# Optimization experiments

Hardware: AMD Instinct MI355X
Metric: run time of the kernel (lower is better)

The kernel has to match this reference:

```python
import jax, jax.numpy as jnp
import numpy as np

N0, N1, N2 = 1500, 6000, 4000
F_IN, F_OUT = 32, 32
K00, K0P = 2, 2
K1N, K11, K12, K1P = 2, 2, 2, 2
K2N, K22 = 2, 2


def chebyshev(L, k, x):
    # Chebyshev recursion: T1 = L x, T2 = 2 L T1 - x, T_j = 2 L T_{j-1} - T_{j-2}
    # Returns (n, F, k) stack of T1..Tk (identity term handled by caller).
    t_prev = L @ x
    terms = [t_prev]
    t_pp = x
    for _ in range(k - 1):
        t = 2.0 * (L @ t_prev) - t_pp
        t_pp, t_prev = t_prev, t
        terms.append(t)
    return jnp.stack(terms, axis=2)


def _sym(key, n):
    a = jax.random.normal(key, (n, n), jnp.float32) / jnp.sqrt(jnp.float32(n))
    return 0.5 * (a + a.T)


def setup_inputs():
    key = jax.random.key(0)
    ks = jax.random.split(key, 16)
    x0 = jax.random.normal(ks[0], (N0, F_IN), jnp.float32)
    x1 = jax.random.normal(ks[1], (N1, F_IN), jnp.float32)
    x2 = jax.random.normal(ks[2], (N2, F_IN), jnp.float32)
    B1 = jax.random.normal(ks[3], (N0, N1), jnp.float32) / jnp.sqrt(jnp.float32(N1))
    B2 = jax.random.normal(ks[4], (N1, N2), jnp.float32) / jnp.sqrt(jnp.float32(N2))
    L0 = _sym(ks[5], N0)
    L1l = _sym(ks[6], N1)
    L1u = _sym(ks[7], N1)
    L2 = _sym(ks[8], N2)
    # Degree matrices: diagonal with strictly positive entries (as in real SC data).
    D1 = jnp.diag(jax.random.uniform(ks[9], (N0,), jnp.float32, 0.5, 2.0))
    D2 = jnp.diag(jax.random.uniform(ks[10], (N1,), jnp.float32, 0.5, 2.0))
    D3 = jnp.diag(jax.random.uniform(ks[11], (N2,), jnp.float32, 0.5, 2.0))
    D5 = jnp.diag(jax.random.uniform(ks[12], (N1,), jnp.float32, 0.5, 2.0))
    W0 = jax.random.normal(ks[13], (F_IN, F_OUT, 1 + K00 + 1 + K0P), jnp.float32) * 0.05
    W1 = jax.random.normal(ks[14], (F_IN, F_OUT, 1 + K1N + 1 + K11 + K12 + 1 + K1P), jnp.float32) * 0.05
    W2 = jax.random.normal(ks[15], (F_IN, F_OUT, 1 + K2N + 1 + K22), jnp.float32) * 0.05
    return dict(x0=x0, x1=x1, x2=x2, B1=B1, B2=B2, L0=L0, L1l=L1l, L1u=L1u,
                L2=L2, D1=D1, D2=D2, D3=D3, D5=D5, W0=W0, W1=W1, W2=W2)


def _forward(x0, x1, x2, B1, B2, L0, L1l, L1u, L2, d1_inv, d2, d3, d5_pinv, W0, W1, W2):
    # ---- order 0 ----
    x0p = d1_inv[:, None] * (B1 @ x1)               # inv(D1) @ B1 @ x1
    X0 = jnp.concatenate([x0[:, :, None], chebyshev(L0, K00, x0),
                          x0p[:, :, None], chebyshev(L0, K0P, x0p)], axis=2)
    # ---- order 1 ----
    x1n = d2[:, None] * (B1.T @ (d1_inv[:, None] * x0))  # D2 @ B1.T @ inv(D1) @ x0
    x1p = B2 @ (d3[:, None] * x2)                        # B2 @ D3 @ x2
    X1 = jnp.concatenate([x1n[:, :, None], chebyshev(L1l, K1N, x1n),
                          x1[:, :, None], chebyshev(L1l, K11, x1), chebyshev(L1u, K12, x1),
                          x1p[:, :, None], chebyshev(L1u, K1P, x1p)], axis=2)
    # ---- order 2 ----
    x2n = B2.T @ (d5_pinv[:, None] * x1)                 # B2.T @ pinv(D5) @ x1
    X2 = jnp.concatenate([x2n[:, :, None], chebyshev(L2, K2N, x2n),
                          x2[:, :, None], chebyshev(L2, K22, x2)], axis=2)
    y0 = jax.nn.relu(jnp.einsum('nik,iok->no', X0, W0))
    y1 = jax.nn.relu(jnp.einsum('nik,iok->no', X1, W1))
    y2 = jax.nn.relu(jnp.einsum('nik,iok->no', X2, W2))
    return (y0, y1, y2)


def reference(x0, x1, x2, B1, B2, L0, L1l, L1u, L2, D1, D2, D3, D5, W0, W1, W2):
    # D matrices are diagonal degree matrices; inverse/pinverse of a diagonal
    # matrix is the diagonal of (safe) reciprocals -- identical math to
    # torch.inverse / torch.pinverse on these inputs, without an O(n^3) solve.
    d1_inv = 1.0 / jnp.diag(D1)
    d2 = jnp.diag(D2)
    d3 = jnp.diag(D3)
    d5 = jnp.diag(D5)
    d5_pinv = jnp.where(d5 != 0, 1.0 / d5, 0.0)
    return _forward(x0, x1, x2, B1, B2, L0, L1l, L1u, L2, d1_inv, d2, d3, d5_pinv, W0, W1, W2)
```

## Files before the change

### kernel.cpp

```cpp
#include <hip/hip_runtime.h>
#include <stdint.h>

typedef __attribute__((ext_vector_type(4))) float f32x4;
typedef __attribute__((ext_vector_type(8))) short s16x8;
typedef unsigned short us;

static __device__ __forceinline__ us f2bf(float f) {
  union { float f; uint32_t u; } v; v.f = f;
  uint32_t u = v.u;
  u += 0x7fffu + ((u >> 16) & 1u);
  return (us)(u >> 16);
}

static __device__ __forceinline__ float dval(const float* dv, long r, long dstr, int mode) {
  if (!dv || mode == 0) return 1.f;
  float d = dv[r * dstr];
  if (mode == 2) return (d != 0.f) ? 1.f / d : 0.f;
  return d;
}

static __device__ void tpose_tile(const float* __restrict__ src, long lds_, int n,
                                  const float* __restrict__ dv, long dstr, int mode,
                                  us* __restrict__ dst, int ldn, int tile,
                                  us (*sm)[72]) {
  const int t = threadIdx.x;
  const int r0 = tile * 64;
  {
    const int rr = t & 63;
    const int cg = t >> 6;
    const int gr = r0 + rr;
    float sc = 1.f;
    f32x4 v0 = {0.f, 0.f, 0.f, 0.f}, v1 = {0.f, 0.f, 0.f, 0.f};
    if (gr < n) {
      sc = dval(dv, gr, dstr, mode);
      const float* sp = src + (long)gr * lds_ + cg * 8;
      v0 = *(const f32x4*)sp;
      v1 = *(const f32x4*)(sp + 4);
    }
#pragma unroll
    for (int j = 0; j < 4; ++j) {
      sm[cg * 8 + j][rr] = f2bf(v0[j] * sc);
      sm[cg * 8 + 4 + j][rr] = f2bf(v1[j] * sc);
    }
  }
  __syncthreads();
  {
    const int f = t >> 3;
    const int nc = (t & 7) * 8;
    if (r0 + nc < ldn) {
      s16x8 v = *(const s16x8*)&sm[f][nc];
      *(s16x8*)(dst + (size_t)f * ldn + r0 + nc) = v;
    }
  }
}

static __device__ void convT_tile(const float* __restrict__ in, int ldi, int nI, int nC,
                                  us* __restrict__ outT, int ldoT, int bx, int by,
                                  us (*sT)[72]) {
  const int t = threadIdx.x;
  const int tc0 = bx * 64;
  const int tr0 = by * 64;
  const int c0 = (t & 15) * 4;
  const int r0 = (t >> 4) * 4;
  us ub[4][4];
#pragma unroll
  for (int j = 0; j < 4; ++j) {
    int gr = tr0 + r0 + j;
    f32x4 v = {0.f, 0.f, 0.f, 0.f};
    if (gr < nI) {
      const float* pI = in + (size_t)gr * ldi + tc0 + c0;
      if (tc0 + c0 + 3 < nC) {
        v = *(const f32x4*)pI;
      } else {
#pragma unroll
        for (int jj = 0; jj < 4; ++jj) if (tc0 + c0 + jj < nC) v[jj] = pI[jj];
      }
    }
#pragma unroll
    for (int jj = 0; jj < 4; ++jj) ub[j][jj] = f2bf(v[jj]);
  }
#pragma unroll
  for (int jj = 0; jj < 4; ++jj) {
    union { us u[4]; unsigned long long ll; } w;
#pragma unroll
    for (int j = 0; j < 4; ++j) w.u[j] = ub[j][jj];
    *(unsigned long long*)&sT[c0 + jj][r0] = w.ll;
  }
  __syncthreads();
#pragma unroll
  for (int p = 0; p < 2; ++p) {
    int orow = (t >> 3) + p * 32;
    int rcol = (t & 7) * 8;
    int grow = tc0 + orow;
    int gcol = tr0 + rcol;
    if (grow < nC && gcol < ldoT) {
      union { unsigned long long ll[2]; s16x8 v; } w;
      w.ll[0] = *(const unsigned long long*)&sT[orow][rcol];
      w.ll[1] = *(const unsigned long long*)&sT[orow][rcol + 4];
      *(s16x8*)(outT + (size_t)grow * ldoT + gcol) = w.v;
    }
  }
}

struct TSeg { const float* src; us* dst; int lds_, n, ldn, start; };
struct TPack { TSeg t[8]; int nseg; };

__global__ __launch_bounds__(256) void tpose_batch(TPack P) {
  __shared__ us sm[32][72];
  int b = blockIdx.x;
  int si = P.nseg - 1;
  while (si > 0 && P.t[si].start > b) --si;
  const TSeg s = P.t[si];
  tpose_tile(s.src, s.lds_, s.n, nullptr, 0, 0, s.dst, s.ldn, b - s.start, sm);
}

__global__ __launch_bounds__(256) void prep(
    const float* __restrict__ x0, const float* __restrict__ x1, const float* __restrict__ x2,
    const float* __restrict__ D1, const float* __restrict__ D3, const float* __restrict__ D5,
    const float* __restrict__ W0, const float* __restrict__ W1, const float* __restrict__ W2,
    us* x0T, us* x0dT, us* x1T, us* x1dT, us* x2T, us* x2dT,
    us* W0T, us* W1T, us* W2T,
    float* __restrict__ X0a, float* __restrict__ X1a, float* __restrict__ X2a) {
  __shared__ us sm[32][72];
  int b = blockIdx.x;
  if (b < 24)  { tpose_tile(x0, 32, 1500, nullptr, 0, 0, x0T, 1536, b, sm); return; }
  b -= 24;
  if (b < 24)  { tpose_tile(x0, 32, 1500, D1, 1501, 2, x0dT, 1536, b, sm); return; }
  b -= 24;
  if (b < 94)  { tpose_tile(x1, 32, 6000, nullptr, 0, 0, x1T, 6016, b, sm); return; }
  b -= 94;
  if (b < 94)  { tpose_tile(x1, 32, 6000, D5, 6001, 2, x1dT, 6016, b, sm); return; }
  b -= 94;
  if (b < 63)  { tpose_tile(x2, 32, 4000, nullptr, 0, 0, x2T, 4032, b, sm); return; }
  b -= 63;
  if (b < 63)  { tpose_tile(x2, 32, 4000, D3, 4001, 1, x2dT, 4032, b, sm); return; }
  b -= 63;
  if (b < 3) {
    const float* W = (b == 0) ? W0 : ((b == 1) ? W1 : W2);
    us* dst = (b == 0) ? W0T : ((b == 1) ? W1T : W2T);
    const int K = (b == 1) ? 11 : 6;
    const int C = K * 32;
    const int CP = (b == 1) ? 384 : 192;
    for (int idx = threadIdx.x; idx < 32 * CP; idx += 256) {
      int o = idx / CP, j = idx - o * CP;
      float v = 0.f;
      if (j < C) { int k = j >> 5, i = j & 31; v = W[((long)i * 32 + o) * K + k]; }
      dst[(size_t)o * CP + j] = f2bf(v);
    }
    return;
  }
  b -= 3;
  const long V0 = 1500L * 48, V1 = 6000L * 88, V2 = 4000L * 48;
  for (long i = (long)b * 256 + threadIdx.x; i < V0 + V1 + V2; i += 512L * 256) {
    f32x4 v = {0.f, 0.f, 0.f, 0.f};
    float* dst;
    if (i < V0) {
      long r = i / 48; int c0 = (int)(i - r * 48) * 4;
      if (c0 < 32) v = *(const f32x4*)(x0 + r * 32 + c0);
      dst = X0a + r * 192 + c0;
    } else if (i < V0 + V1) {
      long j = i - V0; long r = j / 88; int c0 = (int)(j - r * 88) * 4;
      if (c0 >= 96 && c0 < 128) v = *(const f32x4*)(x1 + r * 32 + (c0 - 96));
      dst = X1a + r * 352 + c0;
    } else {
      long j = i - V0 - V1; long r = j / 48; int c0 = (int)(j - r * 48) * 4;
      if (c0 >= 96 && c0 < 128) v = *(const f32x4*)(x2 + r * 32 + (c0 - 96));
      dst = X2a + r * 192 + c0;
    }
    *(f32x4*)dst = v;
  }
}

struct Seg {
  const void* A; us* Aout;
  const us* Bt0; const us* Bt1;
  const float* S0; const float* S1; const float* sv;
  float* C0; float* C1;
  float alpha, beta;
  int lda, ldao, ldS, sstr, ldc;
  int n_rows, n_k, ldb, smode, kchunk, tiles, ky, start;
};
struct CSeg { const float* in; us* out; int ldi, nI, nC, ldoT, cx, start; };
struct Mega {
  Seg s[4]; CSeg c[2]; TSeg t[2];
  int nseg, gemm_end, nconv, conv_end, ntp;
};

template <int F, bool RELU, typename AT>
__global__ __launch_bounds__(256) void mega(Mega P) {
  __shared__ __align__(16) us lds[64 * 128];
  const int b = blockIdx.x;
  if (b >= P.gemm_end) {
    if (b < P.conv_end) {
      int lb = b - P.gemm_end;
      int si = P.nconv - 1;
      while (si > 0 && P.c[si].start > lb) --si;
      const CSeg s = P.c[si];
      int l = lb - s.start;
      convT_tile(s.in, s.ldi, s.nI, s.nC, s.out, s.ldoT, l % s.cx, l / s.cx, (us(*)[72])lds);
    } else {
      int lb = b - P.conv_end;
      int si = P.ntp - 1;
      while (si > 0 && P.t[si].start > lb) --si;
      const TSeg s = P.t[si];
      tpose_tile(s.src, s.lds_, s.n, nullptr, 0, 0, s.dst, s.ldn, lb - s.start, (us(*)[72])lds);
    }
    return;
  }

  us* sA = lds;
  us* sX = lds + 64 * 64;

  int si = P.nseg - 1;
  while (si > 0 && P.s[si].start > b) --si;
  const Seg sg = P.s[si];
  const int local = b - sg.start;
  const int bx = local % sg.tiles;
  const int kidx = local / sg.tiles;

  const AT* __restrict__ A = (const AT*)sg.A;
  const int n_rows = sg.n_rows, n_k = sg.n_k, ldb = sg.ldb;

  const int tid = threadIdx.x;
  const int k_begin = kidx * sg.kchunk;
  const int k_end = min(n_k, k_begin + sg.kchunk);
  const int nsteps = (k_end - k_begin + 63) >> 6;

  const int srow = tid >> 2;
  const int sslot = tid & 3;
  const int kc_off = sslot * 16;
  const long arowg = (long)bx * 64 + srow;
  const bool arow_ok = arowg < n_rows;
  const bool xrow_ok = (F == 64) || (srow < 32);
  const us* xbase = ((srow < 32) ? sg.Bt0 : sg.Bt1) + (size_t)(srow & 31) * ldb;

  s16x8 abf0 = (s16x8)0, abf1 = (s16x8)0;
  f32x4 af0, af1, af2, af3;
  s16x8 x0r = (s16x8)0, x1r = (s16x8)0;

  auto load_tiles = [&](int k0) {
    int kc = k0 + kc_off;
    if constexpr (sizeof(AT) == 4) {
      af0 = f32x4{0, 0, 0, 0}; af1 = af0; af2 = af0; af3 = af0;
      if (arow_ok) {
        const float* ap = (const float*)A + (size_t)arowg * sg.lda + kc;
        if (kc + 15 < n_k) {
          af0 = *(const f32x4*)ap; af1 = *(const f32x4*)(ap + 4);
          af2 = *(const f32x4*)(ap + 8); af3 = *(const f32x4*)(ap + 12);
        } else {
#pragma unroll
          for (int j = 0; j < 4; ++j) {
            if (kc + j < n_k) af0[j] = ap[j];
            if (kc + 4 + j < n_k) af1[j] = ap[4 + j];
            if (kc + 8 + j < n_k) af2[j] = ap[8 + j];
            if (kc + 12 + j < n_k) af3[j] = ap[12 + j];
          }
        }
      }
    } else {
      abf0 = (s16x8)0; abf1 = (s16x8)0;
      if (arow_ok) {
        const us* ap = (const us*)A + (size_t)arowg * sg.lda + kc;
        if (kc + 15 < n_k) {
          abf0 = *(const s16x8*)ap; abf1 = *(const s16x8*)(ap + 8);
        } else {
#pragma unroll
          for (int j = 0; j < 8; ++j) {
            if (kc + j < n_k) abf0[j] = (short)ap[j];
            if (kc + 8 + j < n_k) abf1[j] = (short)ap[8 + j];
          }
        }
      }
    }
    if (xrow_ok) {
      x0r = *(const s16x8*)(xbase + kc);
      x1r = *(const s16x8*)(xbase + kc + 8);
    }
  };

  load_tiles(k_begin);

  const int wave = tid >> 6;
  const int lane = tid & 63;
  const int g = lane >> 4;
  const int r = lane & 15;
  const int wslot0 = ((2 * sslot) ^ (srow & 7)) * 8;
  const int wslot1 = ((2 * sslot + 1) ^ (srow & 7)) * 8;

  f32x4 acc[F / 16];
#pragma unroll
  for (int i = 0; i < F / 16; ++i) acc[i] = f32x4{0.f, 0.f, 0.f, 0.f};

  for (int s = 0; s < nsteps; ++s) {
    s16x8 pk0, pk1;
    if constexpr (sizeof(AT) == 4) {
#pragma unroll
      for (int j = 0; j < 4; ++j) {
        pk0[j] = (short)f2bf(af0[j]); pk0[4 + j] = (short)f2bf(af1[j]);
        pk1[j] = (short)f2bf(af2[j]); pk1[4 + j] = (short)f2bf(af3[j]);
      }
      if (sg.Aout && arow_ok) {
        us* q = sg.Aout + (size_t)arowg * sg.ldao + (k_begin + s * 64 + kc_off);
        *(s16x8*)q = pk0;
        *(s16x8*)(q + 8) = pk1;
      }
    } else { pk0 = abf0; pk1 = abf1; }
    *(s16x8*)&sA[srow * 64 + wslot0] = pk0;
    *(s16x8*)&sA[srow * 64 + wslot1] = pk1;
    if (xrow_ok) {
      *(s16x8*)&sX[srow * 64 + wslot0] = x0r;
      *(s16x8*)&sX[srow * 64 + wslot1] = x1r;
    }
    __syncthreads();
    if (s + 1 < nsteps) load_tiles(k_begin + (s + 1) * 64);

    const int arow = wave * 16 + r;
#pragma unroll
    for (int kk = 0; kk < 2; ++kk) {
      s16x8 afr = *(s16x8*)&sA[arow * 64 + (((kk * 4 + g) ^ (arow & 7)) << 3)];
#pragma unroll
      for (int nt = 0; nt < F / 16; ++nt) {
        int xc = nt * 16 + r;
        s16x8 bfr = *(s16x8*)&sX[xc * 64 + (((kk * 4 + g) ^ (xc & 7)) << 3)];
        acc[nt] = __builtin_amdgcn_mfma_f32_16x16x32_bf16(afr, bfr, acc[nt], 0, 0, 0);
      }
    }
    __syncthreads();
  }

  float svv[4];
#pragma unroll
  for (int j = 0; j < 4; ++j) {
    long row = (long)bx * 64 + wave * 16 + g * 4 + j;
    svv[j] = (row < n_rows) ? dval(sg.sv, row, sg.sstr, sg.smode) : 0.f;
  }
#pragma unroll
  for (int nt = 0; nt < F / 16; ++nt) {
    float* C = (F == 64 && nt >= 2) ? sg.C1 : sg.C0;
    const float* S = (F == 64 && nt >= 2) ? sg.S1 : sg.S0;
    int col = ((F == 64) ? (nt & 1) : nt) * 16 + r;
#pragma unroll
    for (int j = 0; j < 4; ++j) {
      long row = (long)bx * 64 + wave * 16 + g * 4 + j;
      if (row < n_rows) {
        float v = sg.alpha * acc[nt][j] * svv[j];
        if (S && (sg.ky == 1 || kidx == 0)) v += sg.beta * S[row * (size_t)sg.ldS + col];
        if (sg.ky > 1) {
          atomicAdd(&C[row * (size_t)sg.ldc + col], v);
        } else {
          if (RELU) v = fmaxf(v, 0.0f);
          C[row * (size_t)sg.ldc + col] = v;
        }
      }
    }
  }
}

__global__ void colcopy(float* __restrict__ dst, const float* __restrict__ src, int n,
                        const float* __restrict__ dv, long dstr, int mode) {
  int idx = blockIdx.x * 256 + threadIdx.x;
  if (idx >= n * 32) return;
  dst[idx] = src[idx] * dval(dv, idx >> 5, dstr, mode);
}
__global__ void scale_ld(float* __restrict__ dst, long ld, int n,
                         const float* __restrict__ dv, long dstr, int mode) {
  int idx = blockIdx.x * 256 + threadIdx.x;
  if (idx >= n * 32) return;
  dst[(size_t)(idx >> 5) * ld + (idx & 31)] *= dval(dv, idx >> 5, dstr, mode);
}
__global__ __launch_bounds__(256) void mm_at(
    const float* __restrict__ A, int lda, int m,
    const float* __restrict__ X,
    float* __restrict__ C, int ldc, int n, int kchunk) {
  const int fg = threadIdx.x & 3;
  const int cg = threadIdx.x >> 2;
  const int c = blockIdx.x * 256 + cg * 4;
  const int k0 = blockIdx.y * kchunk;
  const int k1 = min(m, k0 + kchunk);
  const int f = fg * 8;
  float acc[4][8];
#pragma unroll
  for (int a = 0; a < 4; ++a)
#pragma unroll
    for (int b = 0; b < 8; ++b) acc[a][b] = 0.f;
  for (int k = k0; k < k1; ++k) {
    const float* Ar = A + (size_t)k * lda + c;
    f32x4 a;
    if (c + 3 < n) a = *(const f32x4*)Ar;
    else {
      a = f32x4{0.f, 0.f, 0.f, 0.f};
#pragma unroll
      for (int j = 0; j < 4; ++j) if (c + j < n) a[j] = Ar[j];
    }
    f32x4 xa = *(const f32x4*)(X + (size_t)k * 32 + f);
    f32x4 xb = *(const f32x4*)(X + (size_t)k * 32 + f + 4);
#pragma unroll
    for (int cc = 0; cc < 4; ++cc)
#pragma unroll
      for (int jj = 0; jj < 4; ++jj) {
        acc[cc][jj] += a[cc] * xa[jj];
        acc[cc][4 + jj] += a[cc] * xb[jj];
      }
  }
  if (c >= n) return;
#pragma unroll
  for (int cc = 0; cc < 4; ++cc) {
    if (c + cc >= n) break;
#pragma unroll
    for (int jj = 0; jj < 8; ++jj)
      atomicAdd(&C[(size_t)(c + cc) * ldc + f + jj], acc[cc][jj]);
  }
}


extern "C" void kernel_launch(void* const* d_in, const int* in_sizes, int n_in,
                              void* d_out, int out_size, void* d_ws, size_t ws_size,
                              hipStream_t stream) {
  (void)in_sizes; (void)n_in; (void)out_size;
  const float* x0  = (const float*)d_in[0];
  const float* x1  = (const float*)d_in[1];
  const float* x2  = (const float*)d_in[2];
  const float* B1  = (const float*)d_in[3];
  const float* B2  = (const float*)d_in[4];
  const float* L0  = (const float*)d_in[5];
  const float* L1l = (const float*)d_in[6];
  const float* L1u = (const float*)d_in[7];
  const float* L2  = (const float*)d_in[8];
  const float* D1  = (const float*)d_in[9];
  const float* D2  = (const float*)d_in[10];
  const float* D3  = (const float*)d_in[11];
  const float* D5  = (const float*)d_in[12];
  const float* W0  = (const float*)d_in[13];
  const float* W1  = (const float*)d_in[14];
  const float* W2  = (const float*)d_in[15];
  float* out = (float*)d_out;

  char* p = (char*)d_ws;
  auto alloc = [&](size_t b) { char* r = p; p += (b + 255) & ~(size_t)255; return r; };

  us* x0T   = (us*)alloc((size_t)32 * 1536 * 2);
  us* x0dT  = (us*)alloc((size_t)32 * 1536 * 2);
  us* x1T   = (us*)alloc((size_t)32 * 6016 * 2);
  us* x1dT  = (us*)alloc((size_t)32 * 6016 * 2);
  us* x2T   = (us*)alloc((size_t)32 * 4032 * 2);
  us* x2dT  = (us*)alloc((size_t)32 * 4032 * 2);
  us* x0pT  = (us*)alloc((size_t)32 * 1536 * 2);
  us* x1nT  = (us*)alloc((size_t)32 * 6016 * 2);
  us* x1pT  = (us*)alloc((size_t)32 * 6016 * 2);
  us* x2nT  = (us*)alloc((size_t)32 * 4032 * 2);
  us* T1a0T = (us*)alloc((size_t)32 * 1536 * 2);
  us* T1b0T = (us*)alloc((size_t)32 * 1536 * 2);
  us* T1laT = (us*)alloc((size_t)32 * 6016 * 2);
  us* T1lbT = (us*)alloc((size_t)32 * 6016 * 2);
  us* T1uaT = (us*)alloc((size_t)32 * 6016 * 2);
  us* T1ubT = (us*)alloc((size_t)32 * 6016 * 2);
  us* T1a2T = (us*)alloc((size_t)32 * 4032 * 2);
  us* T1b2T = (us*)alloc((size_t)32 * 4032 * 2);
  us* W0T   = (us*)alloc((size_t)32 * 192 * 2);
  us* W1T   = (us*)alloc((size_t)32 * 384 * 2);
  us* W2T   = (us*)alloc((size_t)32 * 192 * 2);

  float* X0a = (float*)alloc((size_t)1500 * 192 * 4);
  float* X1a = (float*)alloc((size_t)6000 * 352 * 4);
  float* X2a = (float*)alloc((size_t)4000 * 192 * 4);

  float* z0  = (float*)alloc((size_t)1500 * 32 * 4);
  float* sx1 = (float*)alloc((size_t)6000 * 32 * 4);

  size_t used = (size_t)(p - (char*)d_ws);
  const size_t needB  = (size_t)6000 * 1536 * 2 + (size_t)4000 * 6016 * 2 + 1024;
  const size_t needL1 = 2 * (size_t)6000 * 6016 * 2 + 1024;
  const size_t needL02 = (size_t)1500 * 1536 * 2 + (size_t)4000 * 4032 * 2 + 1024;
  bool haveB = used + needB <= ws_size;
  int tier = 0;
  if (haveB) {
    if (used + needB + needL1 + needL02 <= ws_size) tier = 2;
    else if (used + needB + needL1 <= ws_size) tier = 1;
  }
  us *B1t = nullptr, *B2t = nullptr;
  us *L0bf = nullptr, *L1lbf = nullptr, *L1ubf = nullptr, *L2bf = nullptr;
  if (haveB) {
    B1t = (us*)alloc((size_t)6000 * 1536 * 2);
    B2t = (us*)alloc((size_t)4000 * 6016 * 2);
  }
  if (tier >= 1) {
    L1lbf = (us*)alloc((size_t)6000 * 6016 * 2);
    L1ubf = (us*)alloc((size_t)6000 * 6016 * 2);
  }
  if (tier >= 2) {
    L0bf = (us*)alloc((size_t)1500 * 1536 * 2);
    L2bf = (us*)alloc((size_t)4000 * 4032 * 2);
  }

  auto nb = [](long t) { return (unsigned)((t + 255) / 256); };
  auto seg = [](const void* A, us* Aout, int lda, int ldao, int n_rows, int n_k,
                const us* Bt0, const us* Bt1, int ldb,
                float alpha, const float* S0, const float* S1, int ldS, float beta,
                const float* sv, int sstr, int smode,
                float* C0, float* C1, int ldc,
                int kchunk, int tiles, int ky, int start) {
    Seg s;
    s.A = A; s.Aout = Aout; s.Bt0 = Bt0; s.Bt1 = Bt1; s.S0 = S0; s.S1 = S1; s.sv = sv;
    s.C0 = C0; s.C1 = C1; s.alpha = alpha; s.beta = beta;
    s.lda = lda; s.ldao = ldao; s.ldS = ldS; s.sstr = sstr; s.ldc = ldc;
    s.n_rows = n_rows; s.n_k = n_k; s.ldb = ldb; s.smode = smode;
    s.kchunk = kchunk; s.tiles = tiles; s.ky = ky; s.start = start;
    return s;
  };

  prep<<<877, 256, 0, stream>>>(x0, x1, x2, D1, D3, D5, W0, W1, W2,
                                x0T, x0dT, x1T, x1dT, x2T, x2dT, W0T, W1T, W2T,
                                X0a, X1a, X2a);

  {
    Mega P{};
    P.nseg = 2;
    P.s[0] = seg(B1, nullptr, 6000, 0, 1500, 6000, x1T, x1T, 6016,
                 1.f, nullptr, nullptr, 0, 0.f, D1, 1501, 2,
                 X0a + 3 * 32, nullptr, 192, 768, 24, 8, 0);
    P.s[1] = seg(B2, nullptr, 4000, 0, 6000, 4000, x2dT, x2dT, 4032,
                 1.f, nullptr, nullptr, 0, 0.f, nullptr, 0, 0,
                 X1a + 8 * 32, nullptr, 352, 512, 94, 8, 192);
    P.gemm_end = 944;
    if (haveB) {
      P.nconv = 2;
      P.c[0] = CSeg{B1, B1t, 6000, 1500, 6000, 1536, 94, 0};
      P.c[1] = CSeg{B2, B2t, 4000, 6000, 4000, 6016, 63, 2256};
      P.conv_end = 944 + 8178;
    } else {
      P.nconv = 0; P.conv_end = 944;
    }
    P.ntp = 0;
    mega<32, false, float><<<P.conv_end, 256, 0, stream>>>(P);
  }

  if (haveB) {
    Mega P{};
    P.nseg = 2;
    P.s[0] = seg(B1t, nullptr, 1536, 0, 6000, 1536, x0dT, x0dT, 1536,
                 1.f, nullptr, nullptr, 0, 0.f, D2, 6001, 1,
                 X1a + 0 * 32, nullptr, 352, 384, 94, 4, 0);
    P.s[1] = seg(B2t, nullptr, 6016, 0, 4000, 6016, x1dT, x1dT, 6016,
                 1.f, nullptr, nullptr, 0, 0.f, nullptr, 0, 0,
                 X2a + 0 * 32, nullptr, 192, 768, 63, 8, 376);
    P.gemm_end = 880;
    P.nconv = 0; P.conv_end = 880;
    P.ntp = 2;
    P.t[0] = TSeg{X0a + 3 * 32, x0pT, 192, 1500, 1536, 0};
    P.t[1] = TSeg{X1a + 8 * 32, x1pT, 352, 6000, 6016, 24};
    mega<32, false, us><<<998, 256, 0, stream>>>(P);
  } else {
    colcopy<<<nb(1500L * 32), 256, 0, stream>>>(z0, x0, 1500, D1, 1501, 2);
    mm_at<<<dim3(24, 24), 256, 0, stream>>>(B1, 6000, 1500, z0, X1a + 0 * 32, 352, 6000, 63);
    scale_ld<<<nb(6000L * 32), 256, 0, stream>>>(X1a + 0 * 32, 352, 6000, D2, 6001, 1);
    colcopy<<<nb(6000L * 32), 256, 0, stream>>>(sx1, x1, 6000, D5, 6001, 2);
    mm_at<<<dim3(16, 32), 256, 0, stream>>>(B2, 4000, 6000, sx1, X2a + 0 * 32, 192, 4000, 188);
    TPack T{};
    T.nseg = 2;
    T.t[0] = TSeg{X0a + 3 * 32, x0pT, 192, 1500, 1536, 0};
    T.t[1] = TSeg{X1a + 8 * 32, x1pT, 352, 6000, 6016, 24};
    tpose_batch<<<118, 256, 0, stream>>>(T);
  }

  {
    TPack T{};
    T.nseg = 2;
    T.t[0] = TSeg{X1a + 0 * 32, x1nT, 352, 6000, 6016, 0};
    T.t[1] = TSeg{X2a + 0 * 32, x2nT, 192, 4000, 4032, 94};
    tpose_batch<<<157, 256, 0, stream>>>(T);
  }

  {
    Mega P{};
    P.nseg = 4;
    P.s[0] = seg(L0, L0bf, 1500, 1536, 1500, 1500, x0T, x0pT, 1536,
                 1.f, nullptr, nullptr, 0, 0.f, nullptr, 0, 0,
                 X0a + 1 * 32, X0a + 4 * 32, 192, 384, 24, 4, 0);
    P.s[1] = seg(L1l, L1lbf, 6000, 6016, 6000, 6000, x1nT, x1T, 6016,
                 1.f, nullptr, nullptr, 0, 0.f, nullptr, 0, 0,
                 X1a + 1 * 32, X1a + 4 * 32, 352, 768, 94, 8, 96);
    P.s[2] = seg(L1u, L1ubf, 6000, 6016, 6000, 6000, x1T, x1pT, 6016,
                 1.f, nullptr, nullptr, 0, 0.f, nullptr, 0, 0,
                 X1a + 6 * 32, X1a + 9 * 32, 352, 768, 94, 8, 848);
    P.s[3] = seg(L2, L2bf, 4000, 4032, 4000, 4000, x2nT, x2T, 4032,
                 1.f, nullptr, nullptr, 0, 0.f, nullptr, 0, 0,
                 X2a + 1 * 32, X2a + 4 * 32, 192, 512, 63, 8, 1600);
    P.gemm_end = 2104; P.nconv = 0; P.conv_end = 2104; P.ntp = 0;
    mega<64, false, float><<<2104, 256, 0, stream>>>(P);
  }

  {
    TPack T{};
    T.nseg = 8;
    T.t[0] = TSeg{X0a + 1 * 32, T1a0T, 192, 1500, 1536, 0};
    T.t[1] = TSeg{X0a + 4 * 32, T1b0T, 192, 1500, 1536, 24};
    T.t[2] = TSeg{X1a + 1 * 32, T1laT, 352, 6000, 6016, 48};
    T.t[3] = TSeg{X1a + 4 * 32, T1lbT, 352, 6000, 6016, 142};
    T.t[4] = TSeg{X1a + 6 * 32, T1uaT, 352, 6000, 6016, 236};
    T.t[5] = TSeg{X1a + 9 * 32, T1ubT, 352, 6000, 6016, 330};
    T.t[6] = TSeg{X2a + 1 * 32, T1a2T, 192, 4000, 4032, 424};
    T.t[7] = TSeg{X2a + 4 * 32, T1b2T, 192, 4000, 4032, 487};
    tpose_batch<<<550, 256, 0, stream>>>(T);
  }

  {
    if (tier == 2) {
      Mega P{};
      P.nseg = 4;
      P.s[0] = seg(L0bf, nullptr, 1536, 0, 1500, 1536, T1a0T, T1b0T, 1536,
                   2.f, X0a + 0 * 32, X0a + 3 * 32, 192, -1.f, nullptr, 0, 0,
                   X0a + 2 * 32, X0a + 5 * 32, 192, 384, 24, 4, 0);
      P.s[1] = seg(L1lbf, nullptr, 6016, 0, 6000, 6016, T1laT, T1lbT, 6016,
                   2.f, X1a + 0 * 32, X1a + 3 * 32, 352, -1.f, nullptr, 0, 0,
                   X1a + 2 * 32, X1a + 5 * 32, 352, 768, 94, 8, 96);
      P.s[2] = seg(L1ubf, nullptr, 6016, 0, 6000, 6016, T1uaT, T1ubT, 6016,
                   2.f, X1a + 3 * 32, X1a + 8 * 32, 352, -1.f, nullptr, 0, 0,
                   X1a + 7 * 32, X1a + 10 * 32, 352, 768, 94, 8, 848);
      P.s[3] = seg(L2bf, nullptr, 4032, 0, 4000, 4032, T1a2T, T1b2T, 4032,
                   2.f, X2a + 0 * 32, X2a + 3 * 32, 192, -1.f, nullptr, 0, 0,
                   X2a + 2 * 32, X2a + 5 * 32, 192, 512, 63, 8, 1600);
      P.gemm_end = 2104; P.nconv = 0; P.conv_end = 2104; P.ntp = 0;
      mega<64, false, us><<<2104, 256, 0, stream>>>(P);
    } else if (tier == 1) {
      Mega P{};
      P.nseg = 2;
      P.s[0] = seg(L1lbf, nullptr, 6016, 0, 6000, 6016, T1laT, T1lbT, 6016,
                   2.f, X1a + 0 * 32, X1a + 3 * 32, 352, -1.f, nullptr, 0, 0,
                   X1a + 2 * 32, X1a + 5 * 32, 352, 768, 94, 8, 0);
      P.s[1] = seg(L1ubf, nullptr, 6016, 0, 6000, 6016, T1uaT, T1ubT, 6016,
                   2.f, X1a + 3 * 32, X1a + 8 * 32, 352, -1.f, nullptr, 0, 0,
                   X1a + 7 * 32, X1a + 10 * 32, 352, 768, 94, 8, 752);
      P.gemm_end = 1504; P.nconv = 0; P.conv_end = 1504; P.ntp = 0;
      mega<64, false, us><<<1504, 256, 0, stream>>>(P);
      Mega Q{};
      Q.nseg = 2;
      Q.s[0] = seg(L0, nullptr, 1500, 0, 1500, 1500, T1a0T, T1b0T, 1536,
                   2.f, X0a + 0 * 32, X0a + 3 * 32, 192, -1.f, nullptr, 0, 0,
                   X0a + 2 * 32, X0a + 5 * 32, 192, 384, 24, 4, 0);
      Q.s[1] = seg(L2, nullptr, 4000, 0, 4000, 4000, T1a2T, T1b2T, 4032,
                   2.f, X2a + 0 * 32, X2a + 3 * 32, 192, -1.f, nullptr, 0, 0,
                   X2a + 2 * 32, X2a + 5 * 32, 192, 512, 63, 8, 96);
      Q.gemm_end = 600; Q.nconv = 0; Q.conv_end = 600; Q.ntp = 0;
      mega<64, false, float><<<600, 256, 0, stream>>>(Q);
    } else {
      Mega P{};
      P.nseg = 4;
      P.s[0] = seg(L0, nullptr, 1500, 0, 1500, 1500, T1a0T, T1b0T, 1536,
                   2.f, X0a + 0 * 32, X0a + 3 * 32, 192, -1.f, nullptr, 0, 0,
                   X0a + 2 * 32, X0a + 5 * 32, 192, 384, 24, 4, 0);
      P.s[1] = seg(L1l, nullptr, 6000, 0, 6000, 6000, T1laT, T1lbT, 6016,
                   2.f, X1a + 0 * 32, X1a + 3 * 32, 352, -1.f, nullptr, 0, 0,
                   X1a + 2 * 32, X1a + 5 * 32, 352, 768, 94, 8, 96);
      P.s[2] = seg(L1u, nullptr, 6000, 0, 6000, 6000, T1uaT, T1ubT, 6016,
                   2.f, X1a + 3 * 32, X1a + 8 * 32, 352, -1.f, nullptr, 0, 0,
                   X1a + 7 * 32, X1a + 10 * 32, 352, 768, 94, 8, 848);
      P.s[3] = seg(L2, nullptr, 4000, 0, 4000, 4000, T1a2T, T1b2T, 4032,
                   2.f, X2a + 0 * 32, X2a + 3 * 32, 192, -1.f, nullptr, 0, 0,
                   X2a + 2 * 32, X2a + 5 * 32, 192, 512, 63, 8, 1600);
      P.gemm_end = 2104; P.nconv = 0; P.conv_end = 2104; P.ntp = 0;
      mega<64, false, float><<<2104, 256, 0, stream>>>(P);
    }
  }

  {
    Mega P{};
    P.nseg = 3;
    P.s[0] = seg(X0a, nullptr, 192, 0, 1500, 192, W0T, W0T, 192,
                 1.f, nullptr, nullptr, 0, 0.f, nullptr, 0, 0,
                 out, nullptr, 32, 192, 24, 1, 0);
    P.s[1] = seg(X1a, nullptr, 352, 0, 6000, 352, W1T, W1T, 384,
                 1.f, nullptr, nullptr, 0, 0.f, nullptr, 0, 0,
                 out + 48000, nullptr, 32, 384, 94, 1, 24);
    P.s[2] = seg(X2a, nullptr, 192, 0, 4000, 192, W2T, W2T, 192,
                 1.f, nullptr, nullptr, 0, 0.f, nullptr, 0, 0,
                 out + 240000, nullptr, 32, 192, 63, 1, 118);
    P.gemm_end = 181; P.nconv = 0; P.conv_end = 181; P.ntp = 0;
    mega<32, true, float><<<181, 256, 0, stream>>>(P);
  }
}
```

Before: 315.7 us.

## Drop bf16 Laplacian caching and halve split-K in Chebyshev GEMMs

Removes the path that wrote bf16 copies of the Laplacians during the first Chebyshev pass and reread them in the second. Both passes now read the fp32 Laplacians directly. This cuts the extra global writes in the first pass but doubles the bytes read in the second. The split-K chunks for the Laplacian GEMMs are also doubled (ky halved), roughly halving grid size and the partial-sum traffic.

```diff
diff --git a/kernel.cpp b/kernel.cpp
--- a/kernel.cpp
+++ b/kernel.cpp
@@ -172,12 +172,12 @@
 }
 
 struct Seg {
-  const void* A; us* Aout;
+  const void* A;
   const us* Bt0; const us* Bt1;
   const float* S0; const float* S1; const float* sv;
   float* C0; float* C1;
   float alpha, beta;
-  int lda, ldao, ldS, sstr, ldc;
+  int lda, ldS, sstr, ldc;
   int n_rows, n_k, ldb, smode, kchunk, tiles, ky, start;
 };
 struct CSeg { const float* in; us* out; int ldi, nI, nC, ldoT, cx, start; };
@@ -299,11 +299,6 @@
         pk0[j] = (short)f2bf(af0[j]); pk0[4 + j] = (short)f2bf(af1[j]);
         pk1[j] = (short)f2bf(af2[j]); pk1[4 + j] = (short)f2bf(af3[j]);
       }
-      if (sg.Aout && arow_ok) {
-        us* q = sg.Aout + (size_t)arowg * sg.ldao + (k_begin + s * 64 + kc_off);
-        *(s16x8*)q = pk0;
-        *(s16x8*)(q + 8) = pk1;
-      }
     } else { pk0 = abf0; pk1 = abf1; }
     *(s16x8*)&sA[srow * 64 + wslot0] = pk0;
     *(s16x8*)&sA[srow * 64 + wslot1] = pk1;
@@ -382,7 +377,7 @@
 #pragma unroll
   for (int a = 0; a < 4; ++a)
 #pragma unroll
-    for (int b = 0; b < 8; ++b) acc[a][b] = 0.f;
+    for (int bb = 0; bb < 8; ++bb) acc[a][bb] = 0.f;
   for (int k = k0; k < k1; ++k) {
     const float* Ar = A + (size_t)k * lda + c;
     f32x4 a;
@@ -468,41 +463,25 @@
   float* sx1 = (float*)alloc((size_t)6000 * 32 * 4);
 
   size_t used = (size_t)(p - (char*)d_ws);
-  const size_t needB  = (size_t)6000 * 1536 * 2 + (size_t)4000 * 6016 * 2 + 1024;
-  const size_t needL1 = 2 * (size_t)6000 * 6016 * 2 + 1024;
-  const size_t needL02 = (size_t)1500 * 1536 * 2 + (size_t)4000 * 4032 * 2 + 1024;
+  const size_t needB = (size_t)6000 * 1536 * 2 + (size_t)4000 * 6016 * 2 + 1024;
   bool haveB = used + needB <= ws_size;
-  int tier = 0;
-  if (haveB) {
-    if (used + needB + needL1 + needL02 <= ws_size) tier = 2;
-    else if (used + needB + needL1 <= ws_size) tier = 1;
-  }
   us *B1t = nullptr, *B2t = nullptr;
-  us *L0bf = nullptr, *L1lbf = nullptr, *L1ubf = nullptr, *L2bf = nullptr;
   if (haveB) {
     B1t = (us*)alloc((size_t)6000 * 1536 * 2);
     B2t = (us*)alloc((size_t)4000 * 6016 * 2);
   }
-  if (tier >= 1) {
-    L1lbf = (us*)alloc((size_t)6000 * 6016 * 2);
-    L1ubf = (us*)alloc((size_t)6000 * 6016 * 2);
-  }
-  if (tier >= 2) {
-    L0bf = (us*)alloc((size_t)1500 * 1536 * 2);
-    L2bf = (us*)alloc((size_t)4000 * 4032 * 2);
-  }
 
   auto nb = [](long t) { return (unsigned)((t + 255) / 256); };
-  auto seg = [](const void* A, us* Aout, int lda, int ldao, int n_rows, int n_k,
+  auto seg = [](const void* A, int lda, int n_rows, int n_k,
                 const us* Bt0, const us* Bt1, int ldb,
                 float alpha, const float* S0, const float* S1, int ldS, float beta,
                 const float* sv, int sstr, int smode,
                 float* C0, float* C1, int ldc,
                 int kchunk, int tiles, int ky, int start) {
     Seg s;
-    s.A = A; s.Aout = Aout; s.Bt0 = Bt0; s.Bt1 = Bt1; s.S0 = S0; s.S1 = S1; s.sv = sv;
+    s.A = A; s.Bt0 = Bt0; s.Bt1 = Bt1; s.S0 = S0; s.S1 = S1; s.sv = sv;
     s.C0 = C0; s.C1 = C1; s.alpha = alpha; s.beta = beta;
-    s.lda = lda; s.ldao = ldao; s.ldS = ldS; s.sstr = sstr; s.ldc = ldc;
+    s.lda = lda; s.ldS = ldS; s.sstr = sstr; s.ldc = ldc;
     s.n_rows = n_rows; s.n_k = n_k; s.ldb = ldb; s.smode = smode;
     s.kchunk = kchunk; s.tiles = tiles; s.ky = ky; s.start = start;
     return s;
@@ -515,10 +494,10 @@
   {
     Mega P{};
     P.nseg = 2;
-    P.s[0] = seg(B1, nullptr, 6000, 0, 1500, 6000, x1T, x1T, 6016,
+    P.s[0] = seg(B1, 6000, 1500, 6000, x1T, x1T, 6016,
                  1.f, nullptr, nullptr, 0, 0.f, D1, 1501, 2,
                  X0a + 3 * 32, nullptr, 192, 768, 24, 8, 0);
-    P.s[1] = seg(B2, nullptr, 4000, 0, 6000, 4000, x2dT, x2dT, 4032,
+    P.s[1] = seg(B2, 4000, 6000, 4000, x2dT, x2dT, 4032,
                  1.f, nullptr, nullptr, 0, 0.f, nullptr, 0, 0,
                  X1a + 8 * 32, nullptr, 352, 512, 94, 8, 192);
     P.gemm_end = 944;
@@ -537,10 +516,10 @@
   if (haveB) {
     Mega P{};
     P.nseg = 2;
-    P.s[0] = seg(B1t, nullptr, 1536, 0, 6000, 1536, x0dT, x0dT, 1536,
+    P.s[0] = seg(B1t, 1536, 6000, 1536, x0dT, x0dT, 1536,
                  1.f, nullptr, nullptr, 0, 0.f, D2, 6001, 1,
                  X1a + 0 * 32, nullptr, 352, 384, 94, 4, 0);
-    P.s[1] = seg(B2t, nullptr, 6016, 0, 4000, 6016, x1dT, x1dT, 6016,
+    P.s[1] = seg(B2t, 6016, 4000, 6016, x1dT, x1dT, 6016,
                  1.f, nullptr, nullptr, 0, 0.f, nullptr, 0, 0,
                  X2a + 0 * 32, nullptr, 192, 768, 63, 8, 376);
     P.gemm_end = 880;
@@ -573,20 +552,20 @@
   {
     Mega P{};
     P.nseg = 4;
-    P.s[0] = seg(L0, L0bf, 1500, 1536, 1500, 1500, x0T, x0pT, 1536,
-                 1.f, nullptr, nullptr, 0, 0.f, nullptr, 0, 0,
-                 X0a + 1 * 32, X0a + 4 * 32, 192, 384, 24, 4, 0);
-    P.s[1] = seg(L1l, L1lbf, 6000, 6016, 6000, 6000, x1nT, x1T, 6016,
-                 1.f, nullptr, nullptr, 0, 0.f, nullptr, 0, 0,
-                 X1a + 1 * 32, X1a + 4 * 32, 352, 768, 94, 8, 96);
-    P.s[2] = seg(L1u, L1ubf, 6000, 6016, 6000, 6000, x1T, x1pT, 6016,
-                 1.f, nullptr, nullptr, 0, 0.f, nullptr, 0, 0,
-                 X1a + 6 * 32, X1a + 9 * 32, 352, 768, 94, 8, 848);
-    P.s[3] = seg(L2, L2bf, 4000, 4032, 4000, 4000, x2nT, x2T, 4032,
-                 1.f, nullptr, nullptr, 0, 0.f, nullptr, 0, 0,
-                 X2a + 1 * 32, X2a + 4 * 32, 192, 512, 63, 8, 1600);
-    P.gemm_end = 2104; P.nconv = 0; P.conv_end = 2104; P.ntp = 0;
-    mega<64, false, float><<<2104, 256, 0, stream>>>(P);
+    P.s[0] = seg(L0, 1500, 1500, 1500, x0T, x0pT, 1536,
+                 1.f, nullptr, nullptr, 0, 0.f, nullptr, 0, 0,
+                 X0a + 1 * 32, X0a + 4 * 32, 192, 768, 24, 2, 0);
+    P.s[1] = seg(L1l, 6000, 6000, 6000, x1nT, x1T, 6016,
+                 1.f, nullptr, nullptr, 0, 0.f, nullptr, 0, 0,
+                 X1a + 1 * 32, X1a + 4 * 32, 352, 1536, 94, 4, 48);
+    P.s[2] = seg(L1u, 6000, 6000, 6000, x1T, x1pT, 6016,
+                 1.f, nullptr, nullptr, 0, 0.f, nullptr, 0, 0,
+                 X1a + 6 * 32, X1a + 9 * 32, 352, 1536, 94, 4, 424);
+    P.s[3] = seg(L2, 4000, 4000, 4000, x2nT, x2T, 4032,
+                 1.f, nullptr, nullptr, 0, 0.f, nullptr, 0, 0,
+                 X2a + 1 * 32, X2a + 4 * 32, 192, 1024, 63, 4, 800);
+    P.gemm_end = 1052; P.nconv = 0; P.conv_end = 1052; P.ntp = 0;
+    mega<64, false, float><<<1052, 256, 0, stream>>>(P);
   }
 
   {
@@ -604,74 +583,34 @@
   }
 
   {
-    if (tier == 2) {
-      Mega P{};
-      P.nseg = 4;
-      P.s[0] = seg(L0bf, nullptr, 1536, 0, 1500, 1536, T1a0T, T1b0T, 1536,
-                   2.f, X0a + 0 * 32, X0a + 3 * 32, 192, -1.f, nullptr, 0, 0,
-                   X0a + 2 * 32, X0a + 5 * 32, 192, 384, 24, 4, 0);
-      P.s[1] = seg(L1lbf, nullptr, 6016, 0, 6000, 6016, T1laT, T1lbT, 6016,
-                   2.f, X1a + 0 * 32, X1a + 3 * 32, 352, -1.f, nullptr, 0, 0,
-                   X1a + 2 * 32, X1a + 5 * 32, 352, 768, 94, 8, 96);
-      P.s[2] = seg(L1ubf, nullptr, 6016, 0, 6000, 6016, T1uaT, T1ubT, 6016,
-                   2.f, X1a + 3 * 32, X1a + 8 * 32, 352, -1.f, nullptr, 0, 0,
-                   X1a + 7 * 32, X1a + 10 * 32, 352, 768, 94, 8, 848);
-      P.s[3] = seg(L2bf, nullptr, 4032, 0, 4000, 4032, T1a2T, T1b2T, 4032,
-                   2.f, X2a + 0 * 32, X2a + 3 * 32, 192, -1.f, nullptr, 0, 0,
-                   X2a + 2 * 32, X2a + 5 * 32, 192, 512, 63, 8, 1600);
-      P.gemm_end = 2104; P.nconv = 0; P.conv_end = 2104; P.ntp = 0;
-      mega<64, false, us><<<2104, 256, 0, stream>>>(P);
-    } else if (tier == 1) {
-      Mega P{};
-      P.nseg = 2;
-      P.s[0] = seg(L1lbf, nullptr, 6016, 0, 6000, 6016, T1laT, T1lbT, 6016,
-                   2.f, X1a + 0 * 32, X1a + 3 * 32, 352, -1.f, nullptr, 0, 0,
-                   X1a + 2 * 32, X1a + 5 * 32, 352, 768, 94, 8, 0);
-      P.s[1] = seg(L1ubf, nullptr, 6016, 0, 6000, 6016, T1uaT, T1ubT, 6016,
-                   2.f, X1a + 3 * 32, X1a + 8 * 32, 352, -1.f, nullptr, 0, 0,
-                   X1a + 7 * 32, X1a + 10 * 32, 352, 768, 94, 8, 752);
-      P.gemm_end = 1504; P.nconv = 0; P.conv_end = 1504; P.ntp = 0;
-      mega<64, false, us><<<1504, 256, 0, stream>>>(P);
-      Mega Q{};
-      Q.nseg = 2;
-      Q.s[0] = seg(L0, nullptr, 1500, 0, 1500, 1500, T1a0T, T1b0T, 1536,
-                   2.f, X0a + 0 * 32, X0a + 3 * 32, 192, -1.f, nullptr, 0, 0,
-                   X0a + 2 * 32, X0a + 5 * 32, 192, 384, 24, 4, 0);
-      Q.s[1] = seg(L2, nullptr, 4000, 0, 4000, 4000, T1a2T, T1b2T, 4032,
-                   2.f, X2a + 0 * 32, X2a + 3 * 32, 192, -1.f, nullptr, 0, 0,
-                   X2a + 2 * 32, X2a + 5 * 32, 192, 512, 63, 8, 96);
-      Q.gemm_end = 600; Q.nconv = 0; Q.conv_end = 600; Q.ntp = 0;
-      mega<64, false, float><<<600, 256, 0, stream>>>(Q);
-    } else {
-      Mega P{};
-      P.nseg = 4;
-      P.s[0] = seg(L0, nullptr, 1500, 0, 1500, 1500, T1a0T, T1b0T, 1536,
-                   2.f, X0a + 0 * 32, X0a + 3 * 32, 192, -1.f, nullptr, 0, 0,
-                   X0a + 2 * 32, X0a + 5 * 32, 192, 384, 24, 4, 0);
-      P.s[1] = seg(L1l, nullptr, 6000, 0, 6000, 6000, T1laT, T1lbT, 6016,
-                   2.f, X1a + 0 * 32, X1a + 3 * 32, 352, -1.f, nullptr, 0, 0,
-                   X1a + 2 * 32, X1a + 5 * 32, 352, 768, 94, 8, 96);
-      P.s[2] = seg(L1u, nullptr, 6000, 0, 6000, 6000, T1uaT, T1ubT, 6016,
-                   2.f, X1a + 3 * 32, X1a + 8 * 32, 352, -1.f, nullptr, 0, 0,
-                   X1a + 7 * 32, X1a + 10 * 32, 352, 768, 94, 8, 848);
-      P.s[3] = seg(L2, nullptr, 4000, 0, 4000, 4000, T1a2T, T1b2T, 4032,
-                   2.f, X2a + 0 * 32, X2a + 3 * 32, 192, -1.f, nullptr, 0, 0,
-                   X2a + 2 * 32, X2a + 5 * 32, 192, 512, 63, 8, 1600);
-      P.gemm_end = 2104; P.nconv = 0; P.conv_end = 2104; P.ntp = 0;
-      mega<64, false, float><<<2104, 256, 0, stream>>>(P);
-    }
+    Mega P{};
+    P.nseg = 4;
+    P.s[0] = seg(L0, 1500, 1500, 1500, T1a0T, T1b0T, 1536,
+                 2.f, X0a + 0 * 32, X0a + 3 * 32, 192, -1.f, nullptr, 0, 0,
+                 X0a + 2 * 32, X0a + 5 * 32, 192, 768, 24, 2, 0);
+    P.s[1] = seg(L1l, 6000, 6000, 6000, T1laT, T1lbT, 6016,
+                 2.f, X1a + 0 * 32, X1a + 3 * 32, 352, -1.f, nullptr, 0, 0,
+                 X1a + 2 * 32, X1a + 5 * 32, 352, 1536, 94, 4, 48);
+    P.s[2] = seg(L1u, 6000, 6000, 6000, T1uaT, T1ubT, 6016,
+                 2.f, X1a + 3 * 32, X1a + 8 * 32, 352, -1.f, nullptr, 0, 0,
+                 X1a + 7 * 32, X1a + 10 * 32, 352, 1536, 94, 4, 424);
+    P.s[3] = seg(L2, 4000, 4000, 4000, T1a2T, T1b2T, 4032,
+                 2.f, X2a + 0 * 32, X2a + 3 * 32, 192, -1.f, nullptr, 0, 0,
+                 X2a + 2 * 32, X2a + 5 * 32, 192, 1024, 63, 4, 800);
+    P.gemm_end = 1052; P.nconv = 0; P.conv_end = 1052; P.ntp = 0;
+    mega<64, false, float><<<1052, 256, 0, stream>>>(P);
   }
 
   {
     Mega P{};
     P.nseg = 3;
-    P.s[0] = seg(X0a, nullptr, 192, 0, 1500, 192, W0T, W0T, 192,
+    P.s[0] = seg(X0a, 192, 1500, 192, W0T, W0T, 192,
                  1.f, nullptr, nullptr, 0, 0.f, nullptr, 0, 0,
                  out, nullptr, 32, 192, 24, 1, 0);
-    P.s[1] = seg(X1a, nullptr, 352, 0, 6000, 352, W1T, W1T, 384,
+    P.s[1] = seg(X1a, 352, 6000, 352, W1T, W1T, 384,
                  1.f, nullptr, nullptr, 0, 0.f, nullptr, 0, 0,
                  out + 48000, nullptr, 32, 384, 94, 1, 24);
-    P.s[2] = seg(X2a, nullptr, 192, 0, 4000, 192, W2T, W2T, 192,
+    P.s[2] = seg(X2a, 192, 4000, 192, W2T, W2T, 192,
                  1.f, nullptr, nullptr, 0, 0.f, nullptr, 0, 0,
                  out + 240000, nullptr, 32, 192, 63, 1, 118);
     P.gemm_end = 181; P.nconv = 0; P.conv_end = 181; P.ntp = 0;
```

After: 308.0 us, median of 2. 1.02x faster.
